# Kernel optimization log

Measured on AMD Instinct MI355X. Metric: run time of the kernel, lower is better.

## Reference

```python
import jax, jax.numpy as jnp
import numpy as np

T = 8192          # nb_territories
H = 4096          # hidden_size
N_ACT = 65536     # number of possible (orig, dest) action pairs
NEG = -1000.0     # fill value for masked-out actions (matches torch code)


def setup_inputs() -> dict:
    key = jax.random.key(0)
    ks = jax.random.split(key, 8)
    inv_sqrt = lambda n: 1.0 / np.sqrt(n)
    return {
        "possible_actions": jax.random.randint(ks[0], (N_ACT, 2), 0, T, dtype=jnp.int64)
            if jax.config.jax_enable_x64 else jax.random.randint(ks[0], (N_ACT, 2), 0, T, dtype=jnp.int32),
        "player_presence_map": jax.random.normal(ks[1], (T,), dtype=jnp.float32),
        "W_in": jax.random.normal(ks[2], (H, T), dtype=jnp.float32) * inv_sqrt(T),
        "b_in": jax.random.normal(ks[3], (H,), dtype=jnp.float32) * inv_sqrt(T),
        "W_orig": jax.random.normal(ks[4], (T, H), dtype=jnp.float32) * inv_sqrt(H),
        "b_orig": jax.random.normal(ks[5], (T,), dtype=jnp.float32) * inv_sqrt(H),
        "W_dest": jax.random.normal(ks[6], (T, H), dtype=jnp.float32) * inv_sqrt(H),
        "b_dest": jax.random.normal(ks[7], (T,), dtype=jnp.float32) * inv_sqrt(H),
    }


def reference(possible_actions, player_presence_map, W_in, b_in, W_orig, b_orig, W_dest, b_dest):
    # tiny MLP: x = tanh(Linear(presence)); torig/tdest heads
    x = jnp.tanh(W_in @ player_presence_map + b_in)          # [H]
    torig = jnp.tanh(W_orig @ x + b_orig)                    # [T]
    tdest = jnp.tanh(W_dest @ x + b_dest)                    # [T]
    emb = jnp.outer(torig, tdest)                            # [T, T]
    # vectorized scatter replaces the python loop over possible_actions
    mask = jnp.zeros((T, T), dtype=emb.dtype)
    mask = mask.at[possible_actions[:, 0], possible_actions[:, 1]].set(1.0)
    emb = jnp.where(mask == 1.0, emb, jnp.asarray(NEG, emb.dtype))
    logits = emb.reshape(1, T * T)                           # [1, T*T]
    return jax.nn.softmax(logits, axis=1)
```

## Files before the change

kernel.cpp:

```cpp
#include <hip/hip_runtime.h>

constexpr int TT   = 8192;
constexpr int HH   = 4096;
constexpr int NACT = 65536;
constexpr int NTH  = 256;

typedef float f32x4 __attribute__((ext_vector_type(4)));

__device__ __forceinline__ float block_reduce(float v, float* s, int t)
{
#pragma unroll
    for (int off = 32; off; off >>= 1) v += __shfl_down(v, off, 64);
    if ((t & 63) == 0) s[t >> 6] = v;
    __syncthreads();
    float r = s[0] + s[1] + s[2] + s[3];
    __syncthreads();
    return r;
}

__global__ __launch_bounds__(256) void k_gemv_in_fill(
    const float* __restrict__ W, const float* __restrict__ p,
    const float* __restrict__ b, float* __restrict__ x, float* __restrict__ out)
{
    const int row = blockIdx.x;
    const int t   = threadIdx.x;
    const float4* __restrict__ Wr = reinterpret_cast<const float4*>(W + (size_t)row * TT);
    const float4* __restrict__ pv = reinterpret_cast<const float4*>(p);
    float acc = 0.f;
#pragma unroll
    for (int i = 0; i < TT / 4 / NTH; ++i) {
        float4 w = Wr[i * NTH + t];
        float4 q = pv[i * NTH + t];
        acc += w.x * q.x + w.y * q.y + w.z * q.z + w.w * q.w;
    }
    __shared__ float s[4];
    float sum = block_reduce(acc, s, t);
    if (t == 0) x[row] = tanhf(sum + b[row]);

    f32x4* __restrict__ o4 = reinterpret_cast<f32x4*>(out);
    const f32x4 z = {0.f, 0.f, 0.f, 0.f};
    const size_t base = (size_t)row * 3072;
#pragma unroll
    for (int i = 0; i < 12; ++i)
        __builtin_nontemporal_store(z, &o4[base + i * NTH + t]);
}

__global__ __launch_bounds__(256) void k_heads_fill(
    const float* __restrict__ Wo, const float* __restrict__ bo,
    const float* __restrict__ Wd, const float* __restrict__ bd,
    const float* __restrict__ x, float* __restrict__ th, float* __restrict__ out)
{
    const int r = blockIdx.x;
    const int t = threadIdx.x;
    const float* W; const float* bb; int rr;
    if (r < TT) { W = Wo; bb = bo; rr = r; }
    else        { W = Wd; bb = bd; rr = r - TT; }
    const float4* __restrict__ Wr = reinterpret_cast<const float4*>(W + (size_t)rr * HH);
    const float4* __restrict__ xv = reinterpret_cast<const float4*>(x);
    float acc = 0.f;
#pragma unroll
    for (int i = 0; i < HH / 4 / NTH; ++i) {
        float4 w = Wr[i * NTH + t];
        float4 q = xv[i * NTH + t];
        acc += w.x * q.x + w.y * q.y + w.z * q.z + w.w * q.w;
    }
    __shared__ float s[4];
    float sum = block_reduce(acc, s, t);
    if (t == 0) th[r] = tanhf(sum + bb[rr]);

    f32x4* __restrict__ o4 = reinterpret_cast<f32x4*>(out);
    const f32x4 z = {0.f, 0.f, 0.f, 0.f};
    __builtin_nontemporal_store(z, &o4[12582912 + (size_t)r * NTH + t]);
}

__global__ __launch_bounds__(256) void k_scatter(
    const int* __restrict__ pa, const float* __restrict__ th,
    float* __restrict__ out, float* __restrict__ partial)
{
    const int i = blockIdx.x * NTH + threadIdx.x;
    const int o = pa[2 * i];
    const int d = pa[2 * i + 1];
    const float v = th[o] * th[TT + d];
    const float u = expf(v - 1.0f);
    float old = atomicExch(out + ((size_t)o * TT + d), u);
    float c = (old == 0.0f) ? u : 0.0f;
    __shared__ float s[4];
    float bc = block_reduce(c, s, threadIdx.x);
    if (threadIdx.x == 0) partial[blockIdx.x] = bc;
}

__global__ __launch_bounds__(256) void k_finalize(
    const int* __restrict__ pa, const float* __restrict__ th,
    const float* __restrict__ partial, float* __restrict__ out)
{
    __shared__ float s[4];
    const float invZ = 1.0f / block_reduce(partial[threadIdx.x], s, threadIdx.x);
    const int i = blockIdx.x * NTH + threadIdx.x;
    const int o = pa[2 * i];
    const int d = pa[2 * i + 1];
    const float v = th[o] * th[TT + d];
    out[(size_t)o * TT + d] = expf(v - 1.0f) * invZ;
}

extern "C" void kernel_launch(void* const* d_in, const int* in_sizes, int n_in,
                              void* d_out, int out_size, void* d_ws, size_t ws_size,
                              hipStream_t stream)
{
    const int*   pa  = (const int*)  d_in[0];
    const float* p   = (const float*)d_in[1];
    const float* Win = (const float*)d_in[2];
    const float* bin = (const float*)d_in[3];
    const float* Wo  = (const float*)d_in[4];
    const float* bo  = (const float*)d_in[5];
    const float* Wd  = (const float*)d_in[6];
    const float* bd  = (const float*)d_in[7];
    float* out = (float*)d_out;

    float* x       = (float*)d_ws;
    float* th      = x + HH;
    float* partial = th + 2 * TT;

    k_gemv_in_fill<<<HH,         NTH, 0, stream>>>(Win, p, bin, x, out);
    k_heads_fill  <<<2 * TT,     NTH, 0, stream>>>(Wo, bo, Wd, bd, x, th, out);
    k_scatter     <<<NACT / NTH, NTH, 0, stream>>>(pa, th, out, partial);
    k_finalize    <<<NACT / NTH, NTH, 0, stream>>>(pa, th, partial, out);
}
```

Before: 128.5 us.

## Fuse scatter and finalize kernels with a grid-wide atomic-counter barrier

Merges the scatter and normalize kernels into one launch. Blocks publish their partial sums, then spin on a global counter (reset in the first kernel) until all 256 blocks arrive, and finally rescale their own slots. This removes one kernel launch and the reloading of indices and the recomputing of exp. It relies on all 256 blocks being co-resident to avoid deadlock. Duplicate indices may also behave differently: each thread now writes its own u*invZ instead of recomputing the same value.

```diff
diff --git a/kernel.cpp b/kernel.cpp
--- a/kernel.cpp
+++ b/kernel.cpp
@@ -20,10 +20,13 @@
 
 __global__ __launch_bounds__(256) void k_gemv_in_fill(
     const float* __restrict__ W, const float* __restrict__ p,
-    const float* __restrict__ b, float* __restrict__ x, float* __restrict__ out)
+    const float* __restrict__ b, float* __restrict__ x, float* __restrict__ out,
+    unsigned int* __restrict__ counter)
 {
     const int row = blockIdx.x;
     const int t   = threadIdx.x;
+    if (row == 0 && t == 0) *counter = 0u;
+
     const float4* __restrict__ Wr = reinterpret_cast<const float4*>(W + (size_t)row * TT);
     const float4* __restrict__ pv = reinterpret_cast<const float4*>(p);
     float acc = 0.f;
@@ -73,33 +76,37 @@
     __builtin_nontemporal_store(z, &o4[12582912 + (size_t)r * NTH + t]);
 }
 
-__global__ __launch_bounds__(256) void k_scatter(
+__global__ __launch_bounds__(256) void k_scatter_finalize(
     const int* __restrict__ pa, const float* __restrict__ th,
-    float* __restrict__ out, float* __restrict__ partial)
+    float* __restrict__ out, float* __restrict__ partial,
+    unsigned int* __restrict__ counter)
 {
-    const int i = blockIdx.x * NTH + threadIdx.x;
+    const int b = blockIdx.x;
+    const int t = threadIdx.x;
+    const int i = b * NTH + t;
     const int o = pa[2 * i];
     const int d = pa[2 * i + 1];
+    float* slot = out + ((size_t)o * TT + d);
     const float v = th[o] * th[TT + d];
     const float u = expf(v - 1.0f);
-    float old = atomicExch(out + ((size_t)o * TT + d), u);
+    float old = atomicExch(slot, u);
     float c = (old == 0.0f) ? u : 0.0f;
+
     __shared__ float s[4];
-    float bc = block_reduce(c, s, threadIdx.x);
-    if (threadIdx.x == 0) partial[blockIdx.x] = bc;
-}
+    float bc = block_reduce(c, s, t);
 
-__global__ __launch_bounds__(256) void k_finalize(
-    const int* __restrict__ pa, const float* __restrict__ th,
-    const float* __restrict__ partial, float* __restrict__ out)
-{
-    __shared__ float s[4];
-    const float invZ = 1.0f / block_reduce(partial[threadIdx.x], s, threadIdx.x);
-    const int i = blockIdx.x * NTH + threadIdx.x;
-    const int o = pa[2 * i];
-    const int d = pa[2 * i + 1];
-    const float v = th[o] * th[TT + d];
-    out[(size_t)o * TT + d] = expf(v - 1.0f) * invZ;
+    if (t == 0) {
+        __hip_atomic_store(&partial[b], bc, __ATOMIC_RELEASE, __HIP_MEMORY_SCOPE_AGENT);
+        __atomic_fetch_add(counter, 1u, __ATOMIC_ACQ_REL);
+        while (__hip_atomic_load(counter, __ATOMIC_ACQUIRE, __HIP_MEMORY_SCOPE_AGENT)
+               < (unsigned)gridDim.x)
+            __builtin_amdgcn_s_sleep(8);
+    }
+    __syncthreads();
+
+    float ps = __hip_atomic_load(&partial[t], __ATOMIC_RELAXED, __HIP_MEMORY_SCOPE_AGENT);
+    const float invZ = 1.0f / block_reduce(ps, s, t);
+    *slot = u * invZ;
 }
 
 extern "C" void kernel_launch(void* const* d_in, const int* in_sizes, int n_in,
@@ -116,12 +123,12 @@
     const float* bd  = (const float*)d_in[7];
     float* out = (float*)d_out;
 
-    float* x       = (float*)d_ws;
-    float* th      = x + HH;
-    float* partial = th + 2 * TT;
+    float*        x       = (float*)d_ws;
+    float*        th      = x + HH;
+    float*        partial = th + 2 * TT;
+    unsigned int* counter = (unsigned int*)(partial + 256);
 
-    k_gemv_in_fill<<<HH,         NTH, 0, stream>>>(Win, p, bin, x, out);
-    k_heads_fill  <<<2 * TT,     NTH, 0, stream>>>(Wo, bo, Wd, bd, x, th, out);
-    k_scatter     <<<NACT / NTH, NTH, 0, stream>>>(pa, th, out, partial);
-    k_finalize    <<<NACT / NTH, NTH, 0, stream>>>(pa, th, partial, out);
+    k_gemv_in_fill    <<<HH,         NTH, 0, stream>>>(Win, p, bin, x, out, counter);
+    k_heads_fill      <<<2 * TT,     NTH, 0, stream>>>(Wo, bo, Wd, bd, x, th, out);
+    k_scatter_finalize<<<NACT / NTH, NTH, 0, stream>>>(pa, th, out, partial, counter);
 }
```

New measurement: 142.4 us. +10.8%, slower.
